# Kernel tuning notes

Measured on AMD Instinct MI355X. Metric: run time of the kernel, lower is better.

Reference implementation:

```python
import jax, jax.numpy as jnp
import numpy as np
import math

B, S, D, H, K, V, F, L = 16, 512, 768, 12, 64, 64, 3072, 12
VOCAB, MAXLEN, NTYPE = 30522, 512, 2
EPS = 1e-12


def setup_inputs():
    key = jax.random.key(0)
    ks = iter(jax.random.split(key, 32))
    std = 0.02
    n = lambda shape: jax.random.normal(next(ks), shape, dtype=jnp.float32) * std
    inp = {
        'input_ids': jax.random.randint(next(ks), (B, S), 0, VOCAB, dtype=jnp.int32),
        'attention_mask': jnp.ones((B, S), dtype=jnp.int32),
        'word_emb': n((VOCAB, D)),
        'pos_emb': n((MAXLEN, D)),
        'type_emb': n((NTYPE, D)),
        'emb_ln_w': jnp.ones((D,), jnp.float32),
        'emb_ln_b': jnp.zeros((D,), jnp.float32),
        'Wq': n((L, D, H * K)), 'bq': jnp.zeros((L, H * K), jnp.float32),
        'Wk': n((L, D, H * K)), 'bk': jnp.zeros((L, H * K), jnp.float32),
        'Wv': n((L, D, H * V)), 'bv': jnp.zeros((L, H * V), jnp.float32),
        'Wo': n((L, H * V, D)), 'bo': jnp.zeros((L, D), jnp.float32),
        'ln1_w': jnp.ones((L, D), jnp.float32), 'ln1_b': jnp.zeros((L, D), jnp.float32),
        'Wf1': n((L, D, F)), 'bf1': jnp.zeros((L, F), jnp.float32),
        'Wf2': n((L, F, D)), 'bf2': jnp.zeros((L, D), jnp.float32),
        'ln2_w': jnp.ones((L, D), jnp.float32), 'ln2_b': jnp.zeros((L, D), jnp.float32),
    }
    return inp


def _layernorm(x, w, b):
    m = jnp.mean(x, axis=-1, keepdims=True)
    v = jnp.mean(jnp.square(x - m), axis=-1, keepdims=True)
    return (x - m) * jax.lax.rsqrt(v + EPS) * w + b


def _masked_softmax(a, mask4):
    # exact replica of the custom masked_softmax (multiplicative mask + zero-sum guard)
    mv = a * mask4
    mx = jnp.max(mv, axis=-1, keepdims=True)
    ex = jnp.exp(mv - mx) * mask4
    s = jnp.sum(ex, axis=-1, keepdims=True)
    s = s + (s == 0).astype(s.dtype)
    return ex / s


def _encoder(h, mask4, Wq, bq, Wk, bk, Wv, bv, Wo, bo, ln1_w, ln1_b, Wf1, bf1, Wf2, bf2, ln2_w, ln2_b):
    scale = 1.0 / math.sqrt(K)

    def layer(h, p):
        wq, bq_, wk, bk_, wv, bv_, wo, bo_, l1w, l1b, wf1, bf1_, wf2, bf2_, l2w, l2b = p
        q = (h @ wq + bq_).reshape(B, S, H, K).transpose(0, 2, 1, 3)  # [B,H,S,K]
        k = (h @ wk + bk_).reshape(B, S, H, K).transpose(0, 2, 1, 3)
        v = (h @ wv + bv_).reshape(B, S, H, V).transpose(0, 2, 1, 3)
        a = jnp.einsum('bhqk,bhsk->bhqs', q, k) * scale  # [B,H,S,S]
        a = _masked_softmax(a, mask4)
        o = jnp.einsum('bhqs,bhsv->bhqv', a, v).transpose(0, 2, 1, 3).reshape(B, S, H * V)
        o = o @ wo + bo_
        h1 = _layernorm(h + o, l1w, l1b)
        ff = jax.nn.gelu(h1 @ wf1 + bf1_, approximate=False) @ wf2 + bf2_
        return _layernorm(h1 + ff, l2w, l2b), None

    params = (Wq, bq, Wk, bk, Wv, bv, Wo, bo, ln1_w, ln1_b, Wf1, bf1, Wf2, bf2, ln2_w, ln2_b)
    h, _ = jax.lax.scan(layer, h, params)
    return h


def reference(input_ids, attention_mask, word_emb, pos_emb, type_emb, emb_ln_w, emb_ln_b,
              Wq, bq, Wk, bk, Wv, bv, Wo, bo, ln1_w, ln1_b, Wf1, bf1, Wf2, bf2, ln2_w, ln2_b):
    word = word_emb[input_ids]                      # [B,S,D]
    pos = pos_emb[jnp.arange(S)][None, :, :]        # [1,S,D]
    tok = type_emb[0][None, None, :]                # token_type_ids are all zeros
    h = _layernorm(word + pos + tok, emb_ln_w, emb_ln_b)
    h = jax.lax.stop_gradient(h)  # embeddings computed under torch.no_grad()
    mask4 = attention_mask[:, None, None, :].astype(jnp.float32)
    return _encoder(h, mask4, Wq, bq, Wk, bk, Wv, bv, Wo, bo, ln1_w, ln1_b, Wf1, bf1, Wf2, bf2, ln2_w, ln2_b)
```

## Files before the change

### kernel.cpp

```cpp
#include <hip/hip_runtime.h>
#include <cstdint>
#include <cstddef>

typedef _Float16 f16;
typedef unsigned short u16;
typedef _Float16 f16x8 __attribute__((ext_vector_type(8)));
typedef float f32x4 __attribute__((ext_vector_type(4)));

#define DEV __device__ __forceinline__

DEV float b2f(u16 u) { union { float f; unsigned int i; } x; x.i = ((unsigned int)u) << 16; return x.f; }
DEV u16 f2b(float f) {
  union { float f; unsigned int i; } x; x.f = f;
  unsigned int u = x.i;
  return (u16)((u + 0x7FFFu + ((u >> 16) & 1u)) >> 16);
}
DEV float ldf(const void* p, long i, int isb) {
  return isb ? b2f(((const u16*)p)[i]) : ((const float*)p)[i];
}

DEV void gl_lds16(const f16* g, f16* l) {
  __builtin_amdgcn_global_load_lds((const __attribute__((address_space(1))) void*)g,
                                   (__attribute__((address_space(3))) void*)l, 16, 0, 0);
}

DEV float fast_erf(float x) {
  float ax = fabsf(x);
  float t = __builtin_amdgcn_rcpf(1.f + 0.3275911f * ax);
  float p = t * (0.254829592f + t * (-0.284496736f +
            t * (1.421413741f + t * (-1.453152027f + t * 1.061405429f))));
  float e = 1.f - p * __expf(-ax * ax);
  return copysignf(e, x);
}

__global__ void detect_dtype(const u16* __restrict__ we, int* __restrict__ flag) {
  __shared__ int cnt;
  if (threadIdx.x == 0) cnt = 0;
  __syncthreads();
  int ok = 0;
  for (int i = 0; i < 16; i++) {
    u16 u = we[threadIdx.x * 16 + i];
    int e = (u >> 7) & 0xFF;
    if (e >= 90 && e <= 130) ok++;
  }
  atomicAdd(&cnt, ok);
  __syncthreads();
  if (threadIdx.x == 0) *flag = (cnt > 3481) ? 1 : 0;
}

__global__ __launch_bounds__(256) void transpose_layer(const void* __restrict__ Wq, const void* __restrict__ Wk,
                                                       const void* __restrict__ Wv, const void* __restrict__ Wo,
                                                       const void* __restrict__ Wf1, const void* __restrict__ Wf2,
                                                       f16* __restrict__ wt, int l, const int* __restrict__ dflag) {
  __shared__ f16 tile[32][33];
  int isb = *dflag;
  int bid = blockIdx.x;
  const void* ip;
  f16* op;
  int R, C, rblk, cblk;
  long ioff;
  if (bid < 2304) {
    int which = bid / 576, t = bid % 576;
    R = 768; C = 768;
    cblk = t % 24; rblk = t / 24;
    const void* bases[4] = {Wq, Wk, Wv, Wo};
    ip = bases[which];
    ioff = (long)l * 768 * 768;
    long outs[4] = {0, 589824, 1179648, 1769472};
    op = wt + outs[which];
  } else if (bid < 4608) {
    int t = bid - 2304;
    R = 768; C = 3072;
    cblk = t % 96; rblk = t / 96;
    ip = Wf1; ioff = (long)l * 768 * 3072;
    op = wt + 2359296;
  } else {
    int t = bid - 4608;
    R = 3072; C = 768;
    cblk = t % 24; rblk = t / 24;
    ip = Wf2; ioff = (long)l * 3072 * 768;
    op = wt + 4718592;
  }
  int r0 = rblk * 32, c0 = cblk * 32;
  int tx = threadIdx.x & 31, ty = threadIdx.x >> 5;
  for (int i = 0; i < 4; i++) {
    int r = r0 + ty + 8 * i;
    tile[ty + 8 * i][tx] = (f16)ldf(ip, ioff + (long)r * C + c0 + tx, isb);
  }
  __syncthreads();
  for (int i = 0; i < 4; i++) {
    int c = c0 + ty + 8 * i;
    op[(long)c * R + r0 + tx] = tile[tx][ty + 8 * i];
  }
}

__global__ void prep_bias(const void* bq, const void* bk, const void* bv, const void* bo,
                          const void* bf1, const void* bf2,
                          float* bqkv, float* bo_f, float* bf1f, float* bf2f, const int* dflag) {
  int isb = *dflag;
  int i = blockIdx.x * 256 + threadIdx.x;
  if (i < 12 * 768) {
    int l = i / 768, j = i % 768;
    bqkv[l * 2304 + j] = ldf(bq, i, isb);
    bqkv[l * 2304 + 768 + j] = ldf(bk, i, isb);
    bqkv[l * 2304 + 1536 + j] = ldf(bv, i, isb);
    bo_f[i] = ldf(bo, i, isb);
    bf2f[i] = ldf(bf2, i, isb);
  }
  if (i < 12 * 3072) bf1f[i] = ldf(bf1, i, isb);
}

__global__ __launch_bounds__(256) void embed_ln(const int* __restrict__ ids, const void* __restrict__ we,
                                                const void* __restrict__ pe, const void* __restrict__ te,
                                                const void* __restrict__ lw, const void* __restrict__ lb,
                                                f16* __restrict__ h, const int* __restrict__ dflag) {
  int isb = *dflag;
  int wid = threadIdx.x >> 6, lane = threadIdx.x & 63;
  long t = (long)blockIdx.x * 4 + wid;
  int s = (int)(t & 511);
  long id = ids[t];
  float v[12], s1 = 0.f, s2 = 0.f;
  for (int i = 0; i < 12; i++) {
    int j = i * 64 + lane;
    float f = ldf(we, id * 768 + j, isb) + ldf(pe, (long)s * 768 + j, isb) + ldf(te, j, isb);
    v[i] = f; s1 += f; s2 += f * f;
  }
  for (int d = 1; d < 64; d <<= 1) { s1 += __shfl_xor(s1, d, 64); s2 += __shfl_xor(s2, d, 64); }
  float mean = s1 * (1.f / 768.f);
  float var = fmaxf(s2 * (1.f / 768.f) - mean * mean, 0.f);
  float inv = rsqrtf(var + 1e-12f);
  for (int i = 0; i < 12; i++) {
    int j = i * 64 + lane;
    h[t * 768 + j] = (f16)((v[i] - mean) * inv * ldf(lw, j, isb) + ldf(lb, j, isb));
  }
}

template <int FINAL>
__global__ __launch_bounds__(256) void ln_row(const f16* __restrict__ x, const void* __restrict__ lw,
                                              const void* __restrict__ lb, int l, f16* __restrict__ outf,
                                              void* __restrict__ outg, const int* __restrict__ dflag) {
  int isb = *dflag;
  long poff = (long)l * 768;
  int wid = threadIdx.x >> 6, lane = threadIdx.x & 63;
  long t = (long)blockIdx.x * 4 + wid;
  const f16* xr = x + t * 768;
  float v[12], s1 = 0.f, s2 = 0.f;
  for (int i = 0; i < 12; i++) {
    float f = (float)xr[i * 64 + lane];
    v[i] = f; s1 += f; s2 += f * f;
  }
  for (int d = 1; d < 64; d <<= 1) { s1 += __shfl_xor(s1, d, 64); s2 += __shfl_xor(s2, d, 64); }
  float mean = s1 * (1.f / 768.f);
  float var = fmaxf(s2 * (1.f / 768.f) - mean * mean, 0.f);
  float inv = rsqrtf(var + 1e-12f);
  for (int i = 0; i < 12; i++) {
    int j = i * 64 + lane;
    float o = (v[i] - mean) * inv * ldf(lw, poff + j, isb) + ldf(lb, poff + j, isb);
    long idx = t * 768 + j;
    if (FINAL) {
      if (isb) ((u16*)outg)[idx] = f2b(o);
      else     ((float*)outg)[idx] = o;
    } else {
      outf[idx] = (f16)o;
    }
  }
}

template <int EPI>
__global__ __launch_bounds__(256) void gemm_bt(const f16* __restrict__ A, const f16* __restrict__ Bt,
                                               const float* __restrict__ bias, const f16* __restrict__ resid,
                                               f16* __restrict__ C, int M, int N, int K) {
  __shared__ f16 lA[2][128 * 32];
  __shared__ f16 lB[2][128 * 32];
  int tid = threadIdx.x, lane = tid & 63;
  int wid = tid >> 6;
  int lm = lane & 15, quad = lane >> 4;
  int wm = wid & 1, wn = wid >> 1;

  int gx = gridDim.x;
  int nwg = gx * gridDim.y;
  int flat = blockIdx.y * gx + blockIdx.x;
  int wgid = (flat & 7) * (nwg >> 3) + (flat >> 3);
  long m0 = (long)(wgid / gx) * 128, n0 = (long)(wgid % gx) * 128;

  f32x4 acc[4][4];
  for (int i = 0; i < 4; i++) for (int j = 0; j < 4; j++) acc[i][j] = (f32x4){0.f, 0.f, 0.f, 0.f};

  int srow = lane >> 2;
  int scol = (lane & 3) * 8;
  const f16* ap0 = A + (m0 + wid * 32 + srow) * (long)K + scol;
  const f16* bp0 = Bt + (n0 + wid * 32 + srow) * (long)K + scol;
  long stride16 = 16 * (long)K;

  auto stage = [&](int buf, int kt) {
    f16* la = lA[buf] + wid * 1024;
    f16* lb = lB[buf] + wid * 1024;
    gl_lds16(ap0 + kt, la);
    gl_lds16(ap0 + stride16 + kt, la + 512);
    gl_lds16(bp0 + kt, lb);
    gl_lds16(bp0 + stride16 + kt, lb + 512);
  };

  stage(0, 0);
  int cur = 0;
  for (int kt = 0; kt < K; kt += 32) {
    __syncthreads();
    if (kt + 32 < K) stage(cur ^ 1, kt + 32);
    f16x8 af[4], bf[4];
    for (int mi = 0; mi < 4; mi++) af[mi] = *(const f16x8*)(lA[cur] + (wm * 64 + mi * 16 + lm) * 32 + quad * 8);
    for (int ni = 0; ni < 4; ni++) bf[ni] = *(const f16x8*)(lB[cur] + (wn * 64 + ni * 16 + lm) * 32 + quad * 8);
    for (int mi = 0; mi < 4; mi++)
      for (int ni = 0; ni < 4; ni++)
        acc[mi][ni] = __builtin_amdgcn_mfma_f32_16x16x32_f16(af[mi], bf[ni], acc[mi][ni], 0, 0, 0);
    cur ^= 1;
  }

  for (int mi = 0; mi < 4; mi++)
    for (int ni = 0; ni < 4; ni++) {
      long row = m0 + wm * 64 + mi * 16 + quad * 4;
      long col = n0 + wn * 64 + ni * 16 + lm;
      float bv = bias[col];
      for (int r = 0; r < 4; r++) {
        long idx = (row + r) * N + col;
        float v = acc[mi][ni][r] + bv;
        if (EPI == 1) v = 0.5f * v * (1.f + fast_erf(v * 0.70710678118654752f));
        if (EPI == 2) v += (float)resid[idx];
        C[idx] = (f16)v;
      }
    }
}

__global__ __launch_bounds__(256) void vtrans(const f16* __restrict__ qkv, f16* __restrict__ vT) {
  __shared__ f16 sT[64 * 72];
  int tid = threadIdx.x;
  int st = blockIdx.x, hh = blockIdx.y, bb = blockIdx.z;
  long t0 = (long)bb * 512 + st * 64;
  int r = tid >> 3, c = tid & 7;
  const f16* src = qkv + 1536 + (long)hh * 64 + c * 8;
  *(f16x8*)(sT + r * 72 + c * 8)      = *(const f16x8*)(src + (t0 + r) * 2304);
  *(f16x8*)(sT + (r + 32) * 72 + c * 8) = *(const f16x8*)(src + (t0 + r + 32) * 2304);
  __syncthreads();
  int d = tid >> 2, sq = tid & 3;
  f16 tmp[16];
  for (int j = 0; j < 16; j++) tmp[j] = sT[(sq * 16 + j) * 72 + d];
  f16x8* o = (f16x8*)(vT + ((long)hh * 64 + d) * 8192 + t0 + sq * 16);
  o[0] = *(f16x8*)(tmp);
  o[1] = *(f16x8*)(tmp + 8);
}

__global__ __launch_bounds__(256) void attn_kern(const f16* __restrict__ qkv, const f16* __restrict__ vT,
                                                 const int* __restrict__ amask, f16* __restrict__ out) {
  __shared__ f16 sK[64 * 64];
  __shared__ f16 sVT[64 * 64];
  __shared__ f16 sP[4 * 16 * 72];
  __shared__ float sMall[512];
  int tid = threadIdx.x, wid = tid >> 6, lane = tid & 63;
  int lm = lane & 15, quad = lane >> 4;
  int xb = blockIdx.x, qt = blockIdx.y;
  int hh = xb % 12, bb = xb / 12;
  long tok0 = (long)bb * 512;

  sMall[tid] = (float)amask[tok0 + tid];
  sMall[tid + 256] = (float)amask[tok0 + 256 + tid];

  const f16* qrow = qkv + (tok0 + qt * 64 + wid * 16 + lm) * 2304 + hh * 64;
  f16x8 qa0 = *(const f16x8*)(qrow + quad * 8);
  f16x8 qa1 = *(const f16x8*)(qrow + 32 + quad * 8);
  for (int j = 0; j < 8; j++) {
    qa0[j] = (f16)((float)qa0[j] * 0.125f);
    qa1[j] = (f16)((float)qa1[j] * 0.125f);
  }

  f32x4 oAcc[4];
  float mrun[4], lrun[4];
  for (int r = 0; r < 4; r++) { mrun[r] = -1e30f; lrun[r] = 0.f; }
  for (int vt = 0; vt < 4; vt++) oAcc[vt] = (f32x4){0.f, 0.f, 0.f, 0.f};
  f16* sPw = sP + wid * 16 * 72;
  int swl = (lm & 7) * 8;

  int i0 = wid * 2;
  int key0 = lane >> 3;
  int col = ((lane & 7) ^ (lane >> 3)) * 8;
  const f16* kb0 = qkv + 768 + (long)hh * 64 + col;
  const f16* vb0 = vT + ((long)hh * 64) * 8192 + tok0 + col;

  for (int kt = 0; kt < 8; kt++) {
    long j0 = tok0 + kt * 64;
    __syncthreads();
    for (int ii = 0; ii < 2; ii++) {
      int i = i0 + ii;
      int rowi = i * 8 + key0;
      gl_lds16(kb0 + (j0 + rowi) * 2304, sK + i * 512);
      gl_lds16(vb0 + (long)rowi * 8192 + kt * 64, sVT + i * 512);
    }
    __syncthreads();

    f32x4 sAcc[4];
    for (int nt = 0; nt < 4; nt++) {
      const f16* kr = sK + (nt * 16 + lm) * 64;
      f16x8 b0 = *(const f16x8*)(kr + ((quad * 8) ^ swl));
      f16x8 b1 = *(const f16x8*)(kr + ((32 + quad * 8) ^ swl));
      f32x4 z = (f32x4){0.f, 0.f, 0.f, 0.f};
      z = __builtin_amdgcn_mfma_f32_16x16x32_f16(qa0, b0, z, 0, 0, 0);
      z = __builtin_amdgcn_mfma_f32_16x16x32_f16(qa1, b1, z, 0, 0, 0);
      sAcc[nt] = z;
    }
    float mk[4];
    for (int nt = 0; nt < 4; nt++) mk[nt] = sMall[kt * 64 + nt * 16 + lm];
    float mvv[4][4];
    for (int nt = 0; nt < 4; nt++)
      for (int r = 0; r < 4; r++) mvv[nt][r] = sAcc[nt][r] * mk[nt];
    for (int r = 0; r < 4; r++) {
      float mx = fmaxf(fmaxf(mvv[0][r], mvv[1][r]), fmaxf(mvv[2][r], mvv[3][r]));
      for (int d = 1; d < 16; d <<= 1) mx = fmaxf(mx, __shfl_xor(mx, d, 64));
      float mnew = fmaxf(mrun[r], mx);
      float alpha = __expf(mrun[r] - mnew);
      mrun[r] = mnew;
      float rs = 0.f;
      for (int nt = 0; nt < 4; nt++) {
        float e = __expf(mvv[nt][r] - mnew) * mk[nt];
        rs += e;
        sPw[(quad * 4 + r) * 72 + nt * 16 + lm] = (f16)e;
      }
      for (int d = 1; d < 16; d <<= 1) rs += __shfl_xor(rs, d, 64);
      lrun[r] = lrun[r] * alpha + rs;
      for (int vt = 0; vt < 4; vt++) oAcc[vt][r] *= alpha;
    }
    f16x8 pa0 = *(const f16x8*)(sPw + lm * 72 + quad * 8);
    f16x8 pa1 = *(const f16x8*)(sPw + lm * 72 + 32 + quad * 8);
    for (int vt = 0; vt < 4; vt++) {
      const f16* vr = sVT + (vt * 16 + lm) * 64;
      f16x8 vb0f = *(const f16x8*)(vr + ((quad * 8) ^ swl));
      f16x8 vb1f = *(const f16x8*)(vr + ((32 + quad * 8) ^ swl));
      oAcc[vt] = __builtin_amdgcn_mfma_f32_16x16x32_f16(pa0, vb0f, oAcc[vt], 0, 0, 0);
      oAcc[vt] = __builtin_amdgcn_mfma_f32_16x16x32_f16(pa1, vb1f, oAcc[vt], 0, 0, 0);
    }
  }
  for (int r = 0; r < 4; r++) {
    float l = lrun[r];
    l += (l == 0.f) ? 1.f : 0.f;
    float inv = 1.f / l;
    long row = tok0 + qt * 64 + wid * 16 + quad * 4 + r;
    for (int vt = 0; vt < 4; vt++)
      out[row * 768 + hh * 64 + vt * 16 + lm] = (f16)(oAcc[vt][r] * inv);
  }
}

extern "C" void kernel_launch(void* const* d_in, const int* in_sizes, int n_in,
                              void* d_out, int out_size, void* d_ws, size_t ws_size,
                              hipStream_t stream) {
  const int* ids   = (const int*)d_in[0];
  const int* amask = (const int*)d_in[1];
  const void* we  = d_in[2];
  const void* pe  = d_in[3];
  const void* te  = d_in[4];
  const void* elw = d_in[5];
  const void* elb = d_in[6];
  const void* Wq  = d_in[7];
  const void* bq  = d_in[8];
  const void* Wk  = d_in[9];
  const void* bk  = d_in[10];
  const void* Wv  = d_in[11];
  const void* bv  = d_in[12];
  const void* Wo  = d_in[13];
  const void* bo  = d_in[14];
  const void* l1w = d_in[15];
  const void* l1b = d_in[16];
  const void* Wf1 = d_in[17];
  const void* bf1 = d_in[18];
  const void* Wf2 = d_in[19];
  const void* bf2 = d_in[20];
  const void* l2w = d_in[21];
  const void* l2b = d_in[22];
  (void)in_sizes; (void)n_in; (void)out_size; (void)ws_size;

  char* p = (char*)d_ws;
  auto alloc = [&](size_t bytes) { char* r = p; p += (bytes + 255) & ~(size_t)255; return r; };
  int* dflag  = (int*)alloc(256);
  f16* wt     = (f16*)alloc(9216ll * 768 * 2);
  float* bqkv = (float*)alloc(12 * 2304 * 4);
  float* bo_f = (float*)alloc(12 * 768 * 4);
  float* bf1f = (float*)alloc(12 * 3072 * 4);
  float* bf2f = (float*)alloc(12 * 768 * 4);
  f16* hbuf  = (f16*)alloc(8192ll * 768 * 2);
  f16* h1buf = (f16*)alloc(8192ll * 768 * 2);
  f16* tmp   = (f16*)alloc(8192ll * 768 * 2);
  f16* big   = (f16*)alloc(8192ll * 3072 * 2);
  f16* qkvb  = big;
  f16* ffn1b = big;
  f16* aobuf = big + 8192ll * 2304;

  detect_dtype<<<1, 256, 0, stream>>>((const u16*)we, dflag);
  prep_bias<<<144, 256, 0, stream>>>(bq, bk, bv, bo, bf1, bf2, bqkv, bo_f, bf1f, bf2f, dflag);
  embed_ln<<<2048, 256, 0, stream>>>(ids, we, pe, te, elw, elb, hbuf, dflag);

  for (int l = 0; l < 12; ++l) {
    transpose_layer<<<6912, 256, 0, stream>>>(Wq, Wk, Wv, Wo, Wf1, Wf2, wt, l, dflag);
    gemm_bt<0><<<dim3(18, 64), 256, 0, stream>>>(hbuf, wt, bqkv + l * 2304,
                                                 nullptr, qkvb, 8192, 2304, 768);
    vtrans<<<dim3(8, 12, 16), 256, 0, stream>>>(qkvb, tmp);
    attn_kern<<<dim3(192, 8), 256, 0, stream>>>(qkvb, tmp, amask, aobuf);
    gemm_bt<2><<<dim3(6, 64), 256, 0, stream>>>(aobuf, wt + 1769472, bo_f + l * 768,
                                                hbuf, tmp, 8192, 768, 768);
    ln_row<0><<<2048, 256, 0, stream>>>(tmp, l1w, l1b, l, h1buf, nullptr, dflag);
    gemm_bt<1><<<dim3(24, 64), 256, 0, stream>>>(h1buf, wt + 2359296, bf1f + l * 3072,
                                                 nullptr, ffn1b, 8192, 3072, 768);
    gemm_bt<2><<<dim3(6, 64), 256, 0, stream>>>(ffn1b, wt + 4718592, bf2f + l * 768,
                                                h1buf, tmp, 8192, 768, 3072);
    if (l < 11)
      ln_row<0><<<2048, 256, 0, stream>>>(tmp, l2w, l2b, l, hbuf, nullptr, dflag);
    else
      ln_row<1><<<2048, 256, 0, stream>>>(tmp, l2w, l2b, l, nullptr, d_out, dflag);
  }
}
```

Baseline: 3.707 ms.

## Triple-buffer GEMM K-loop with explicit vmcnt waits and vectorize weight transpose

The GEMM main loop moves from double to triple buffering of the LDS tiles. It uses explicit s_waitcnt vmcnt counts and raw s_barrier so that up to two tile loads stay in flight while MFMA work proceeds. The weight-transpose prep kernel now reads 4 elements per thread with vector loads and writes f16x4 vectors instead of scalar accesses. The risks are more LDS use per block (48KB), which may lower occupancy, and hand-tuned waitcnt values that depend on the compiler not issuing other vector memory ops inside the loop.

```diff
diff --git a/kernel.cpp b/kernel.cpp
--- a/kernel.cpp
+++ b/kernel.cpp
@@ -5,6 +5,7 @@
 typedef _Float16 f16;
 typedef unsigned short u16;
 typedef _Float16 f16x8 __attribute__((ext_vector_type(8)));
+typedef _Float16 f16x4 __attribute__((ext_vector_type(4)));
 typedef float f32x4 __attribute__((ext_vector_type(4)));
 
 #define DEV __device__ __forceinline__
@@ -82,16 +83,26 @@
     op = wt + 4718592;
   }
   int r0 = rblk * 32, c0 = cblk * 32;
-  int tx = threadIdx.x & 31, ty = threadIdx.x >> 5;
-  for (int i = 0; i < 4; i++) {
-    int r = r0 + ty + 8 * i;
-    tile[ty + 8 * i][tx] = (f16)ldf(ip, ioff + (long)r * C + c0 + tx, isb);
+  int tid = threadIdx.x;
+  int row = tid >> 3, cg = (tid & 7) * 4;
+  long base = ioff + (long)(r0 + row) * C + c0 + cg;
+  if (isb) {
+    ushort4 u = *(const ushort4*)((const u16*)ip + base);
+    tile[row][cg + 0] = (f16)b2f(u.x);
+    tile[row][cg + 1] = (f16)b2f(u.y);
+    tile[row][cg + 2] = (f16)b2f(u.z);
+    tile[row][cg + 3] = (f16)b2f(u.w);
+  } else {
+    float4 f = *(const float4*)((const float*)ip + base);
+    tile[row][cg + 0] = (f16)f.x;
+    tile[row][cg + 1] = (f16)f.y;
+    tile[row][cg + 2] = (f16)f.z;
+    tile[row][cg + 3] = (f16)f.w;
   }
   __syncthreads();
-  for (int i = 0; i < 4; i++) {
-    int c = c0 + ty + 8 * i;
-    op[(long)c * R + r0 + tx] = tile[tx][ty + 8 * i];
-  }
+  int col = tid >> 3, rg = (tid & 7) * 4;
+  f16x4 v = (f16x4){tile[rg + 0][col], tile[rg + 1][col], tile[rg + 2][col], tile[rg + 3][col]};
+  *(f16x4*)(op + (long)(c0 + col) * R + r0 + rg) = v;
 }
 
 __global__ void prep_bias(const void* bq, const void* bk, const void* bv, const void* bo,
@@ -170,8 +181,8 @@
 __global__ __launch_bounds__(256) void gemm_bt(const f16* __restrict__ A, const f16* __restrict__ Bt,
                                                const float* __restrict__ bias, const f16* __restrict__ resid,
                                                f16* __restrict__ C, int M, int N, int K) {
-  __shared__ f16 lA[2][128 * 32];
-  __shared__ f16 lB[2][128 * 32];
+  __shared__ f16 lA[3][128 * 32];
+  __shared__ f16 lB[3][128 * 32];
   int tid = threadIdx.x, lane = tid & 63;
   int wid = tid >> 6;
   int lm = lane & 15, quad = lane >> 4;
@@ -201,18 +212,29 @@
     gl_lds16(bp0 + stride16 + kt, lb + 512);
   };
 
+  int nt = K >> 5;
   stage(0, 0);
-  int cur = 0;
-  for (int kt = 0; kt < K; kt += 32) {
-    __syncthreads();
-    if (kt + 32 < K) stage(cur ^ 1, kt + 32);
+  stage(1, 32);
+  stage(2, 64);
+  int cb = 0;
+  for (int t = 0; t < nt; ++t) {
+    int later = nt - 1 - t;
+    if (later >= 2)      asm volatile("s_waitcnt vmcnt(8)" ::: "memory");
+    else if (later == 1) asm volatile("s_waitcnt vmcnt(4)" ::: "memory");
+    else                 asm volatile("s_waitcnt vmcnt(0)" ::: "memory");
+    __builtin_amdgcn_sched_barrier(0);
+    __builtin_amdgcn_s_barrier();
+    const f16* LA = lA[cb];
+    const f16* LB = lB[cb];
     f16x8 af[4], bf[4];
-    for (int mi = 0; mi < 4; mi++) af[mi] = *(const f16x8*)(lA[cur] + (wm * 64 + mi * 16 + lm) * 32 + quad * 8);
-    for (int ni = 0; ni < 4; ni++) bf[ni] = *(const f16x8*)(lB[cur] + (wn * 64 + ni * 16 + lm) * 32 + quad * 8);
+    for (int mi = 0; mi < 4; mi++) af[mi] = *(const f16x8*)(LA + (wm * 64 + mi * 16 + lm) * 32 + quad * 8);
+    for (int ni = 0; ni < 4; ni++) bf[ni] = *(const f16x8*)(LB + (wn * 64 + ni * 16 + lm) * 32 + quad * 8);
     for (int mi = 0; mi < 4; mi++)
       for (int ni = 0; ni < 4; ni++)
         acc[mi][ni] = __builtin_amdgcn_mfma_f32_16x16x32_f16(af[mi], bf[ni], acc[mi][ni], 0, 0, 0);
-    cur ^= 1;
+    __builtin_amdgcn_s_barrier();
+    if (t + 3 < nt) stage(cb, (t + 3) << 5);
+    cb = (cb == 2) ? 0 : cb + 1;
   }
 
   for (int mi = 0; mi < 4; mi++)
```

Result: faster. 3.515 ms (-5.2%).
